# Performance work log

Measured on AMD Instinct MI355X. Metric: run time of the kernel, lower is better.

## Reference

```python
import jax, jax.numpy as jnp
import numpy as np
from jax import lax

B, T, D_IN, D_PROJ, D_OUT, LORDER = 16, 2048, 1024, 512, 1024, 20


def setup_inputs() -> dict:
    key = jax.random.key(0)
    k1, k2, k3, k4 = jax.random.split(key, 4)
    s = 0.05
    return {
        "input": jax.random.normal(k1, (B, T, D_IN), dtype=jnp.float32),
        "in_cache": jnp.zeros((B, D_PROJ, LORDER - 1), dtype=jnp.float32),
        "W_lin": jax.random.normal(k2, (D_IN, D_PROJ), dtype=jnp.float32) * s,
        "conv_w": jax.random.normal(k3, (D_PROJ, LORDER), dtype=jnp.float32) * s,
        "W_aff": jax.random.normal(k4, (D_PROJ, D_OUT), dtype=jnp.float32) * s,
        "b_aff": jnp.zeros((D_OUT,), dtype=jnp.float32),
    }


def reference(input, in_cache, W_lin, conv_w, W_aff, b_aff):
    L = conv_w.shape[1]
    # 1) linear down-projection (no bias): [B,T,Din] -> [B,T,Dp]
    x = jnp.einsum("btd,dp->btp", input, W_lin)
    # 2) FSMN causal depthwise memory block with streaming cache
    xt = jnp.swapaxes(x, 1, 2)                       # [B,Dp,T]
    cat = jnp.concatenate([in_cache, xt], axis=2)    # [B,Dp,T+L-1]
    out_cache = cat[:, :, -(L - 1):]                 # last L-1 frames for next chunk
    # depthwise conv over time, VALID padding -> output length T
    y = lax.conv_general_dilated(
        cat, conv_w[:, None, :],                      # rhs [Dp,1,L]
        window_strides=(1,), padding="VALID",
        dimension_numbers=("NCH", "OIH", "NCH"),
        feature_group_count=conv_w.shape[0])
    m = jnp.swapaxes(y + xt, 1, 2)                   # residual add, back to [B,T,Dp]
    # 3) affine up-projection + 4) ReLU
    out = jax.nn.relu(jnp.einsum("btp,po->bto", m, W_aff) + b_aff)
    return (out, out_cache)
```

## Files before the change

kernel.cpp:

```cpp
#include <hip/hip_runtime.h>
#include <cstdint>
#include <cstddef>

#define B_  16
#define T_  2048
#define DIN 1024
#define DPJ 512
#define DOUT 1024
#define LORD 20
#define HALO (LORD - 1)
#define M_ROWS (B_ * T_)
#define OUT0_ELEMS ((size_t)M_ROWS * DOUT)
#define CACHE_ELEMS ((size_t)B_ * DPJ * (LORD - 1))

typedef __bf16 bf16_t;
typedef __bf16 bf16x2 __attribute__((ext_vector_type(2)));
typedef __bf16 bf16x4 __attribute__((ext_vector_type(4)));
typedef __bf16 bf16x8 __attribute__((ext_vector_type(8)));
typedef float  f32x4  __attribute__((ext_vector_type(4)));

__device__ __forceinline__ void async_load16(const void* g, void* lds_base) {
    __builtin_amdgcn_global_load_lds(
        (const __attribute__((address_space(1))) unsigned int*)g,
        (__attribute__((address_space(3))) unsigned int*)lds_base,
        16, 0, 0);
}

__device__ __forceinline__ int xcd_swizzle(int hw, int nwg) {
    int cpx = nwg >> 3;
    return (hw & 7) * cpx + (hw >> 3);
}

__global__ __launch_bounds__(256) void prep_weights(
    const float* __restrict__ Wl, const float* __restrict__ Wa,
    bf16_t* __restrict__ WlT, bf16_t* __restrict__ WaT) {
    int idx = blockIdx.x * 256 + threadIdx.x;
    const int n1 = DIN * DPJ;
    if (idx < n1) {
        int k = idx / DPJ, n = idx - k * DPJ;
        WlT[(size_t)n * DIN + k] = (bf16_t)Wl[idx];
    } else {
        int j = idx - n1;
        if (j < DPJ * DOUT) {
            int k = j / DOUT, n = j - k * DOUT;
            WaT[(size_t)n * DPJ + k] = (bf16_t)Wa[j];
        }
    }
}

__global__ __launch_bounds__(512, 4) void gemm1_fused(
    const float* __restrict__ A, const bf16_t* __restrict__ Bt,
    bf16_t* __restrict__ C, const int M, const int N, const int K) {
    __shared__ bf16_t sA[128 * 64];
    __shared__ bf16_t sB[128 * 64];

    const int tid  = threadIdx.x;
    const int lane = tid & 63;
    const int wave = tid >> 6;

    const int gx   = gridDim.x;
    const int hw   = blockIdx.y * gx + blockIdx.x;
    const int lid  = xcd_swizzle(hw, gx * gridDim.y);
    const int lby  = lid / gx;
    const int lbx  = lid - lby * gx;
    const int col0 = lbx * 128;
    const int row0 = lby * 128;

    const int s4   = tid & 3;
    const int arow = tid >> 2;
    const float* gA = A + (size_t)(row0 + arow) * K + s4 * 8;
    const int o0 = ((s4       ^ (arow & 7)) << 3);
    const int o1 = (((s4 + 4) ^ (arow & 7)) << 3);
    bf16_t* dst0 = sA + arow * 64;

    const int lr  = lane >> 3;
    const int jsw = (lane & 7) ^ lr;
    const bf16_t* gB0 = Bt + (size_t)(col0 + wave * 16 + lr) * K + jsw * 8;
    bf16_t* lB0 = sB + wave * 1024;

    const int wm = (wave >> 2) * 64;
    const int wn = (wave & 3) * 32;
    const int fr = lane & 15;
    const int fk = lane >> 4;

    const f32x4 zero = {0.f, 0.f, 0.f, 0.f};
    f32x4 acc[4][2];
#pragma unroll
    for (int mt = 0; mt < 4; ++mt)
#pragma unroll
        for (int nt = 0; nt < 2; ++nt) acc[mt][nt] = zero;

    f32x4 g0a, g0b, g0c, g0d;
    g0a = *(const f32x4*)(gA);
    g0b = *(const f32x4*)(gA + 4);
    g0c = *(const f32x4*)(gA + 32);
    g0d = *(const f32x4*)(gA + 36);

    for (int k0 = 0; k0 < K; k0 += 64) {
        asm volatile("s_waitcnt lgkmcnt(0)" ::: "memory");
        __builtin_amdgcn_sched_barrier(0);
        __builtin_amdgcn_s_barrier();
        __builtin_amdgcn_sched_barrier(0);

#pragma unroll
        for (int c = 0; c < 2; ++c)
            async_load16(gB0 + (size_t)c * 8 * K + k0, lB0 + c * 512);

        {
            bf16x8 v0 = { (bf16_t)g0a[0], (bf16_t)g0a[1], (bf16_t)g0a[2], (bf16_t)g0a[3],
                          (bf16_t)g0b[0], (bf16_t)g0b[1], (bf16_t)g0b[2], (bf16_t)g0b[3] };
            bf16x8 v1 = { (bf16_t)g0c[0], (bf16_t)g0c[1], (bf16_t)g0c[2], (bf16_t)g0c[3],
                          (bf16_t)g0d[0], (bf16_t)g0d[1], (bf16_t)g0d[2], (bf16_t)g0d[3] };
            *(bf16x8*)(dst0 + o0) = v0;
            *(bf16x8*)(dst0 + o1) = v1;
        }

        const int kn = k0 + 64;
        if (kn < K) {
            g0a = *(const f32x4*)(gA + kn);
            g0b = *(const f32x4*)(gA + kn + 4);
            g0c = *(const f32x4*)(gA + kn + 32);
            g0d = *(const f32x4*)(gA + kn + 36);
            asm volatile("s_waitcnt vmcnt(4) lgkmcnt(0)" ::: "memory");
        } else {
            asm volatile("s_waitcnt vmcnt(0) lgkmcnt(0)" ::: "memory");
        }
        __builtin_amdgcn_sched_barrier(0);
        __builtin_amdgcn_s_barrier();
        __builtin_amdgcn_sched_barrier(0);

#pragma unroll
        for (int h = 0; h < 2; ++h) {
            bf16x8 af[4], bfr[2];
#pragma unroll
            for (int mt = 0; mt < 4; ++mt) {
                int r = wm + mt * 16 + fr;
                int j = h * 4 + fk;
                af[mt] = *(const bf16x8*)(sA + r * 64 + ((j ^ (r & 7)) << 3));
            }
#pragma unroll
            for (int nt = 0; nt < 2; ++nt) {
                int r = wn + nt * 16 + fr;
                int j = h * 4 + fk;
                bfr[nt] = *(const bf16x8*)(sB + r * 64 + ((j ^ (r & 7)) << 3));
            }
#pragma unroll
            for (int mt = 0; mt < 4; ++mt)
#pragma unroll
                for (int nt = 0; nt < 2; ++nt)
                    acc[mt][nt] = __builtin_amdgcn_mfma_f32_16x16x32_bf16(
                        af[mt], bfr[nt], acc[mt][nt], 0, 0, 0);
        }
    }

    const int er = row0 + wm + (lane >> 4) * 4;
    const int ec = col0 + wn + (lane & 15);
#pragma unroll
    for (int mt = 0; mt < 4; ++mt)
#pragma unroll
        for (int nt = 0; nt < 2; ++nt)
#pragma unroll
            for (int rr = 0; rr < 4; ++rr)
                C[(size_t)(er + mt * 16 + rr) * N + (ec + nt * 16)] =
                    (bf16_t)acc[mt][nt][rr];
}

__global__ __launch_bounds__(512, 4) void gemm_bt_relu(
    const bf16_t* __restrict__ A, const bf16_t* __restrict__ Bt,
    float* __restrict__ C, const float* __restrict__ bias,
    const int M, const int N, const int K) {
    __shared__ bf16_t sA[128 * 64];
    __shared__ bf16_t sB[128 * 64];

    const int tid  = threadIdx.x;
    const int lane = tid & 63;
    const int wave = tid >> 6;

    const int gx   = gridDim.x;
    const int hw   = blockIdx.y * gx + blockIdx.x;
    const int lid  = xcd_swizzle(hw, gx * gridDim.y);
    const int lby  = lid / gx;
    const int lbx  = lid - lby * gx;
    const int col0 = lbx * 128;
    const int row0 = lby * 128;

    const int lr   = lane >> 3;
    const int jsw  = (lane & 7) ^ lr;
    const bf16_t* gA0 = A  + (size_t)(row0 + wave * 16 + lr) * K + jsw * 8;
    const bf16_t* gB0 = Bt + (size_t)(col0 + wave * 16 + lr) * K + jsw * 8;
    bf16_t* lA0 = sA + wave * 1024;
    bf16_t* lB0 = sB + wave * 1024;

    const int wm = (wave >> 2) * 64;
    const int wn = (wave & 3) * 32;
    const int fr = lane & 15;
    const int fk = lane >> 4;

    const f32x4 zero = {0.f, 0.f, 0.f, 0.f};
    f32x4 acc[4][2];
#pragma unroll
    for (int mt = 0; mt < 4; ++mt)
#pragma unroll
        for (int nt = 0; nt < 2; ++nt) acc[mt][nt] = zero;

    for (int k0 = 0; k0 < K; k0 += 64) {
        __syncthreads();
#pragma unroll
        for (int c = 0; c < 2; ++c) {
            async_load16(gA0 + (size_t)c * 8 * K + k0, lA0 + c * 512);
            async_load16(gB0 + (size_t)c * 8 * K + k0, lB0 + c * 512);
        }
        __syncthreads();

#pragma unroll
        for (int h = 0; h < 2; ++h) {
            bf16x8 af[4], bfr[2];
#pragma unroll
            for (int mt = 0; mt < 4; ++mt) {
                int r = wm + mt * 16 + fr;
                int j = h * 4 + fk;
                af[mt] = *(const bf16x8*)(sA + r * 64 + ((j ^ (r & 7)) << 3));
            }
#pragma unroll
            for (int nt = 0; nt < 2; ++nt) {
                int r = wn + nt * 16 + fr;
                int j = h * 4 + fk;
                bfr[nt] = *(const bf16x8*)(sB + r * 64 + ((j ^ (r & 7)) << 3));
            }
#pragma unroll
            for (int mt = 0; mt < 4; ++mt)
#pragma unroll
                for (int nt = 0; nt < 2; ++nt)
                    acc[mt][nt] = __builtin_amdgcn_mfma_f32_16x16x32_bf16(
                        af[mt], bfr[nt], acc[mt][nt], 0, 0, 0);
        }
    }

    const int er = row0 + wm + (lane >> 4) * 4;
    const int ec = col0 + wn + (lane & 15);
#pragma unroll
    for (int nt = 0; nt < 2; ++nt) {
        float bb = bias[ec + nt * 16];
#pragma unroll
        for (int mt = 0; mt < 4; ++mt)
#pragma unroll
            for (int rr = 0; rr < 4; ++rr) {
                float v = acc[mt][nt][rr] + bb;
                C[(size_t)(er + mt * 16 + rr) * N + (ec + nt * 16)] =
                    v > 0.f ? v : 0.f;
            }
    }
}

#define TT 64
#define PPT 128
__global__ __launch_bounds__(256) void dwconv_tiled(
    const bf16_t* __restrict__ x, const float* __restrict__ cache,
    const float* __restrict__ cw, bf16_t* __restrict__ m,
    float* __restrict__ oc) {
    __shared__ float sx[(TT + HALO) * PPT];

    const int tid = threadIdx.x;
    const int t0  = blockIdx.x * TT;
    const int b   = blockIdx.y;
    const int p0  = blockIdx.z * PPT;

    for (int c = tid; c < (TT + HALO) * PPT / 8; c += 256) {
        int r    = c >> 4;
        int col  = (c & 15) << 3;
        int trow = t0 - HALO + r;
        float* dst = sx + r * PPT + col;
        if (trow >= 0) {
            bf16x8 v = *(const bf16x8*)(x + ((size_t)(b * T_ + trow)) * DPJ + p0 + col);
#pragma unroll
            for (int i = 0; i < 8; ++i) dst[i] = (float)v[i];
        } else {
#pragma unroll
            for (int i = 0; i < 8; ++i)
                dst[i] = cache[((size_t)b * DPJ + p0 + col + i) * HALO + (trow + HALO)];
        }
    }
    __syncthreads();

    const int pp   = tid & 63;
    const int half = tid >> 6;
    const int tb   = half * 16;
    const float2* sx2 = (const float2*)sx;

    const int pg = p0 + 2 * pp;
    float2 w[LORD];
#pragma unroll
    for (int l = 0; l < LORD; ++l) {
        w[l].x = cw[pg * LORD + l];
        w[l].y = cw[(pg + 1) * LORD + l];
    }

    float2 win[LORD];
#pragma unroll
    for (int i = 0; i < HALO; ++i) win[i] = sx2[(tb + i) * 64 + pp];

#pragma unroll
    for (int tl = 0; tl < 16; ++tl) {
        float2 nv = sx2[(tb + tl + HALO) * 64 + pp];
        win[(tl + HALO) % LORD] = nv;
        float2 s = nv;
#pragma unroll
        for (int l = 0; l < LORD; ++l) {
            float2 v = win[(tl + l) % LORD];
            s.x += w[l].x * v.x;
            s.y += w[l].y * v.y;
        }
        bf16x2 o = { (bf16_t)s.x, (bf16_t)s.y };
        *(bf16x2*)(m + ((size_t)(b * T_ + t0 + tb + tl)) * DPJ + pg) = o;
    }

    if (blockIdx.x == (T_ / TT) - 1) {
        for (int i = tid; i < PPT * HALO; i += 256) {
            int pl = i / HALO;
            int j  = i - pl * HALO;
            oc[((size_t)b * DPJ + p0 + pl) * HALO + j] = sx[(64 + j) * PPT + pl];
        }
    }
}

extern "C" void kernel_launch(void* const* d_in, const int* in_sizes, int n_in,
                              void* d_out, int out_size, void* d_ws, size_t ws_size,
                              hipStream_t stream) {
    const float* input    = (const float*)d_in[0];
    const float* in_cache = (const float*)d_in[1];
    const float* W_lin    = (const float*)d_in[2];
    const float* conv_w   = (const float*)d_in[3];
    const float* W_aff    = (const float*)d_in[4];
    const float* b_aff    = (const float*)d_in[5];
    float* out = (float*)d_out;

    char* ws = (char*)d_ws;
    bf16_t* x_buf = (bf16_t*)(ws);
    bf16_t* m_buf = (bf16_t*)(ws + 33554432);
    bf16_t* WlinT = (bf16_t*)(ws + 67108864);
    bf16_t* WaffT = (bf16_t*)(ws + 67108864 + 1048576);

    prep_weights<<<(DIN * DPJ + DPJ * DOUT + 255) / 256, 256, 0, stream>>>(
        W_lin, W_aff, WlinT, WaffT);

    gemm1_fused<<<dim3(DPJ / 128, M_ROWS / 128), 512, 0, stream>>>(
        input, WlinT, x_buf, M_ROWS, DPJ, DIN);

    dwconv_tiled<<<dim3(T_ / TT, B_, DPJ / PPT), 256, 0, stream>>>(
        x_buf, in_cache, conv_w, m_buf, out + OUT0_ELEMS);

    gemm_bt_relu<<<dim3(DOUT / 128, M_ROWS / 128), 512, 0, stream>>>(
        m_buf, WaffT, out, b_aff, M_ROWS, DOUT, DPJ);
}
```

Before: 363.8 us.

## Double-buffer LDS in both GEMMs and enlarge per-wave tiles in second GEMM

Both GEMM kernels move to two LDS buffers, so the global-to-LDS staging of the next K tile overlaps the MFMA work on the current one, with one barrier per half-step. The second GEMM drops from 8 to 4 waves per block, each computing a 64x64 sub-tile, which raises register use and per-wave reuse. The weight prep kernel now writes coalesced and reads strided. Doubling LDS to 64KB per block may lower occupancy, and the vmcnt(0) waits in the second GEMM may limit how much overlap it actually gets.

```diff
diff --git a/kernel.cpp b/kernel.cpp
--- a/kernel.cpp
+++ b/kernel.cpp
@@ -37,13 +37,15 @@
     int idx = blockIdx.x * 256 + threadIdx.x;
     const int n1 = DIN * DPJ;
     if (idx < n1) {
-        int k = idx / DPJ, n = idx - k * DPJ;
-        WlT[(size_t)n * DIN + k] = (bf16_t)Wl[idx];
+        int n = idx >> 10;
+        int k = idx - (n << 10);
+        WlT[idx] = (bf16_t)Wl[(size_t)k * DPJ + n];
     } else {
         int j = idx - n1;
         if (j < DPJ * DOUT) {
-            int k = j / DOUT, n = j - k * DOUT;
-            WaT[(size_t)n * DPJ + k] = (bf16_t)Wa[j];
+            int n = j >> 9;
+            int k = j - (n << 9);
+            WaT[j] = (bf16_t)Wa[(size_t)k * DOUT + n];
         }
     }
 }
@@ -51,8 +53,8 @@
 __global__ __launch_bounds__(512, 4) void gemm1_fused(
     const float* __restrict__ A, const bf16_t* __restrict__ Bt,
     bf16_t* __restrict__ C, const int M, const int N, const int K) {
-    __shared__ bf16_t sA[128 * 64];
-    __shared__ bf16_t sB[128 * 64];
+    __shared__ bf16_t sA[2][128 * 64];
+    __shared__ bf16_t sB[2][128 * 64];
 
     const int tid  = threadIdx.x;
     const int lane = tid & 63;
@@ -71,12 +73,10 @@
     const float* gA = A + (size_t)(row0 + arow) * K + s4 * 8;
     const int o0 = ((s4       ^ (arow & 7)) << 3);
     const int o1 = (((s4 + 4) ^ (arow & 7)) << 3);
-    bf16_t* dst0 = sA + arow * 64;
 
     const int lr  = lane >> 3;
     const int jsw = (lane & 7) ^ lr;
     const bf16_t* gB0 = Bt + (size_t)(col0 + wave * 16 + lr) * K + jsw * 8;
-    bf16_t* lB0 = sB + wave * 1024;
 
     const int wm = (wave >> 2) * 64;
     const int wn = (wave & 3) * 32;
@@ -90,45 +90,28 @@
 #pragma unroll
         for (int nt = 0; nt < 2; ++nt) acc[mt][nt] = zero;
 
-    f32x4 g0a, g0b, g0c, g0d;
-    g0a = *(const f32x4*)(gA);
-    g0b = *(const f32x4*)(gA + 4);
-    g0c = *(const f32x4*)(gA + 32);
-    g0d = *(const f32x4*)(gA + 36);
-
-    for (int k0 = 0; k0 < K; k0 += 64) {
-        asm volatile("s_waitcnt lgkmcnt(0)" ::: "memory");
-        __builtin_amdgcn_sched_barrier(0);
-        __builtin_amdgcn_s_barrier();
-        __builtin_amdgcn_sched_barrier(0);
-
+    f32x4 P[4], Q[4];
+
+    auto load_a = [&](f32x4* r, int kk) {
+        r[0] = *(const f32x4*)(gA + kk);
+        r[1] = *(const f32x4*)(gA + kk + 4);
+        r[2] = *(const f32x4*)(gA + kk + 32);
+        r[3] = *(const f32x4*)(gA + kk + 36);
+    };
+    auto cvt_write = [&](const f32x4* r, bf16_t* dstbuf) {
+        bf16x8 v0 = { (bf16_t)r[0][0], (bf16_t)r[0][1], (bf16_t)r[0][2], (bf16_t)r[0][3],
+                      (bf16_t)r[1][0], (bf16_t)r[1][1], (bf16_t)r[1][2], (bf16_t)r[1][3] };
+        bf16x8 v1 = { (bf16_t)r[2][0], (bf16_t)r[2][1], (bf16_t)r[2][2], (bf16_t)r[2][3],
+                      (bf16_t)r[3][0], (bf16_t)r[3][1], (bf16_t)r[3][2], (bf16_t)r[3][3] };
+        *(bf16x8*)(dstbuf + arow * 64 + o0) = v0;
+        *(bf16x8*)(dstbuf + arow * 64 + o1) = v1;
+    };
+    auto stage_b = [&](int kk, bf16_t* dstbuf) {
 #pragma unroll
         for (int c = 0; c < 2; ++c)
-            async_load16(gB0 + (size_t)c * 8 * K + k0, lB0 + c * 512);
-
-        {
-            bf16x8 v0 = { (bf16_t)g0a[0], (bf16_t)g0a[1], (bf16_t)g0a[2], (bf16_t)g0a[3],
-                          (bf16_t)g0b[0], (bf16_t)g0b[1], (bf16_t)g0b[2], (bf16_t)g0b[3] };
-            bf16x8 v1 = { (bf16_t)g0c[0], (bf16_t)g0c[1], (bf16_t)g0c[2], (bf16_t)g0c[3],
-                          (bf16_t)g0d[0], (bf16_t)g0d[1], (bf16_t)g0d[2], (bf16_t)g0d[3] };
-            *(bf16x8*)(dst0 + o0) = v0;
-            *(bf16x8*)(dst0 + o1) = v1;
-        }
-
-        const int kn = k0 + 64;
-        if (kn < K) {
-            g0a = *(const f32x4*)(gA + kn);
-            g0b = *(const f32x4*)(gA + kn + 4);
-            g0c = *(const f32x4*)(gA + kn + 32);
-            g0d = *(const f32x4*)(gA + kn + 36);
-            asm volatile("s_waitcnt vmcnt(4) lgkmcnt(0)" ::: "memory");
-        } else {
-            asm volatile("s_waitcnt vmcnt(0) lgkmcnt(0)" ::: "memory");
-        }
-        __builtin_amdgcn_sched_barrier(0);
-        __builtin_amdgcn_s_barrier();
-        __builtin_amdgcn_sched_barrier(0);
-
+            async_load16(gB0 + (size_t)c * 8 * K + kk, dstbuf + wave * 1024 + c * 512);
+    };
+    auto compute = [&](const bf16_t* bA, const bf16_t* bB) {
 #pragma unroll
         for (int h = 0; h < 2; ++h) {
             bf16x8 af[4], bfr[2];
@@ -136,13 +119,13 @@
             for (int mt = 0; mt < 4; ++mt) {
                 int r = wm + mt * 16 + fr;
                 int j = h * 4 + fk;
-                af[mt] = *(const bf16x8*)(sA + r * 64 + ((j ^ (r & 7)) << 3));
+                af[mt] = *(const bf16x8*)(bA + r * 64 + ((j ^ (r & 7)) << 3));
             }
 #pragma unroll
             for (int nt = 0; nt < 2; ++nt) {
                 int r = wn + nt * 16 + fr;
                 int j = h * 4 + fk;
-                bfr[nt] = *(const bf16x8*)(sB + r * 64 + ((j ^ (r & 7)) << 3));
+                bfr[nt] = *(const bf16x8*)(bB + r * 64 + ((j ^ (r & 7)) << 3));
             }
 #pragma unroll
             for (int mt = 0; mt < 4; ++mt)
@@ -151,6 +134,41 @@
                     acc[mt][nt] = __builtin_amdgcn_mfma_f32_16x16x32_bf16(
                         af[mt], bfr[nt], acc[mt][nt], 0, 0, 0);
         }
+    };
+
+    load_a(P, 0);
+    stage_b(0, sB[0]);
+    cvt_write(P, sA[0]);
+    load_a(P, 64);
+
+    for (int k0 = 0; k0 < K; k0 += 128) {
+        asm volatile("s_waitcnt vmcnt(4) lgkmcnt(0)" ::: "memory");
+        __builtin_amdgcn_sched_barrier(0);
+        __builtin_amdgcn_s_barrier();
+        __builtin_amdgcn_sched_barrier(0);
+        {
+            const int kn = k0 + 64;
+            stage_b(kn, sB[1]);
+            cvt_write(P, sA[1]);
+            if (kn + 64 < K) load_a(Q, kn + 64);
+        }
+        compute(sA[0], sB[0]);
+
+        const int kn2 = k0 + 128;
+        if (kn2 >= K) {
+            asm volatile("s_waitcnt vmcnt(0) lgkmcnt(0)" ::: "memory");
+        } else {
+            asm volatile("s_waitcnt vmcnt(4) lgkmcnt(0)" ::: "memory");
+        }
+        __builtin_amdgcn_sched_barrier(0);
+        __builtin_amdgcn_s_barrier();
+        __builtin_amdgcn_sched_barrier(0);
+        if (kn2 < K) {
+            stage_b(kn2, sB[0]);
+            cvt_write(Q, sA[0]);
+            if (kn2 + 64 < K) load_a(P, kn2 + 64);
+        }
+        compute(sA[1], sB[1]);
     }
 
     const int er = row0 + wm + (lane >> 4) * 4;
@@ -165,12 +183,12 @@
                     (bf16_t)acc[mt][nt][rr];
 }
 
-__global__ __launch_bounds__(512, 4) void gemm_bt_relu(
+__global__ __launch_bounds__(256) void gemm_bt_relu(
     const bf16_t* __restrict__ A, const bf16_t* __restrict__ Bt,
     float* __restrict__ C, const float* __restrict__ bias,
     const int M, const int N, const int K) {
-    __shared__ bf16_t sA[128 * 64];
-    __shared__ bf16_t sB[128 * 64];
+    __shared__ bf16_t sA[2][128 * 64];
+    __shared__ bf16_t sB[2][128 * 64];
 
     const int tid  = threadIdx.x;
     const int lane = tid & 63;
@@ -186,60 +204,76 @@
 
     const int lr   = lane >> 3;
     const int jsw  = (lane & 7) ^ lr;
-    const bf16_t* gA0 = A  + (size_t)(row0 + wave * 16 + lr) * K + jsw * 8;
-    const bf16_t* gB0 = Bt + (size_t)(col0 + wave * 16 + lr) * K + jsw * 8;
-    bf16_t* lA0 = sA + wave * 1024;
-    bf16_t* lB0 = sB + wave * 1024;
-
-    const int wm = (wave >> 2) * 64;
-    const int wn = (wave & 3) * 32;
+    const bf16_t* gA0 = A  + (size_t)(row0 + wave * 32 + lr) * K + jsw * 8;
+    const bf16_t* gB0 = Bt + (size_t)(col0 + wave * 32 + lr) * K + jsw * 8;
+
+    const int wm = (wave >> 1) * 64;
+    const int wn = (wave & 1) * 64;
     const int fr = lane & 15;
     const int fk = lane >> 4;
 
     const f32x4 zero = {0.f, 0.f, 0.f, 0.f};
-    f32x4 acc[4][2];
+    f32x4 acc[4][4];
 #pragma unroll
     for (int mt = 0; mt < 4; ++mt)
 #pragma unroll
-        for (int nt = 0; nt < 2; ++nt) acc[mt][nt] = zero;
-
-    for (int k0 = 0; k0 < K; k0 += 64) {
-        __syncthreads();
-#pragma unroll
-        for (int c = 0; c < 2; ++c) {
-            async_load16(gA0 + (size_t)c * 8 * K + k0, lA0 + c * 512);
-            async_load16(gB0 + (size_t)c * 8 * K + k0, lB0 + c * 512);
-        }
-        __syncthreads();
-
+        for (int nt = 0; nt < 4; ++nt) acc[mt][nt] = zero;
+
+    auto stage = [&](int kk, bf16_t* dA, bf16_t* dB) {
+#pragma unroll
+        for (int c = 0; c < 4; ++c) {
+            async_load16(gA0 + (size_t)c * 8 * K + kk, dA + wave * 2048 + c * 512);
+            async_load16(gB0 + (size_t)c * 8 * K + kk, dB + wave * 2048 + c * 512);
+        }
+    };
+    auto compute = [&](const bf16_t* bA, const bf16_t* bB) {
 #pragma unroll
         for (int h = 0; h < 2; ++h) {
-            bf16x8 af[4], bfr[2];
+            bf16x8 af[4], bfr[4];
 #pragma unroll
             for (int mt = 0; mt < 4; ++mt) {
                 int r = wm + mt * 16 + fr;
                 int j = h * 4 + fk;
-                af[mt] = *(const bf16x8*)(sA + r * 64 + ((j ^ (r & 7)) << 3));
-            }
-#pragma unroll
-            for (int nt = 0; nt < 2; ++nt) {
+                af[mt] = *(const bf16x8*)(bA + r * 64 + ((j ^ (r & 7)) << 3));
+            }
+#pragma unroll
+            for (int nt = 0; nt < 4; ++nt) {
                 int r = wn + nt * 16 + fr;
                 int j = h * 4 + fk;
-                bfr[nt] = *(const bf16x8*)(sB + r * 64 + ((j ^ (r & 7)) << 3));
+                bfr[nt] = *(const bf16x8*)(bB + r * 64 + ((j ^ (r & 7)) << 3));
             }
 #pragma unroll
             for (int mt = 0; mt < 4; ++mt)
 #pragma unroll
-                for (int nt = 0; nt < 2; ++nt)
+                for (int nt = 0; nt < 4; ++nt)
                     acc[mt][nt] = __builtin_amdgcn_mfma_f32_16x16x32_bf16(
                         af[mt], bfr[nt], acc[mt][nt], 0, 0, 0);
         }
+    };
+
+    stage(0, sA[0], sB[0]);
+
+    for (int k0 = 0; k0 < K; k0 += 128) {
+        asm volatile("s_waitcnt vmcnt(0)" ::: "memory");
+        __builtin_amdgcn_sched_barrier(0);
+        __builtin_amdgcn_s_barrier();
+        __builtin_amdgcn_sched_barrier(0);
+        stage(k0 + 64, sA[1], sB[1]);
+        compute(sA[0], sB[0]);
+
+        asm volatile("s_waitcnt vmcnt(0)" ::: "memory");
+        __builtin_amdgcn_sched_barrier(0);
+        __builtin_amdgcn_s_barrier();
+        __builtin_amdgcn_sched_barrier(0);
+        const int kn2 = k0 + 128;
+        if (kn2 < K) stage(kn2, sA[0], sB[0]);
+        compute(sA[1], sB[1]);
     }
 
     const int er = row0 + wm + (lane >> 4) * 4;
     const int ec = col0 + wn + (lane & 15);
 #pragma unroll
-    for (int nt = 0; nt < 2; ++nt) {
+    for (int nt = 0; nt < 4; ++nt) {
         float bb = bias[ec + nt * 16];
 #pragma unroll
         for (int mt = 0; mt < 4; ++mt)
@@ -349,6 +383,6 @@
     dwconv_tiled<<<dim3(T_ / TT, B_, DPJ / PPT), 256, 0, stream>>>(
         x_buf, in_cache, conv_w, m_buf, out + OUT0_ELEMS);
 
-    gemm_bt_relu<<<dim3(DOUT / 128, M_ROWS / 128), 512, 0, stream>>>(
+    gemm_bt_relu<<<dim3(DOUT / 128, M_ROWS / 128), 256, 0, stream>>>(
         m_buf, WaffT, out, b_aff, M_ROWS, DOUT, DPJ);
 }
```

After: 352.4 us. 1.03x faster.
